# Kernel optimization log

Hardware: AMD Instinct MI355X
Metric: run time of the kernel (lower is better)

## Reference

```python
import jax, jax.numpy as jnp
import numpy as np

B, N, NFEAT = 64, 384, 16
E = 3
NHID, NOUT = 128, 128
ST_HID, ST_OUT = 64, 16


def _xavier(key, shape, fan_in, fan_out):
    a = jnp.sqrt(6.0 / (fan_in + fan_out))
    return jax.random.uniform(key, shape, jnp.float32, -a, a)


def setup_inputs() -> dict:
    key = jax.random.key(0)
    ks = jax.random.split(key, 10)
    x = jax.random.normal(ks[0], (B, N, NFEAT), jnp.float32)
    adj = jax.random.uniform(ks[1], (B, E, N, N), jnp.float32)
    emb_w = _xavier(ks[2], (NFEAT, NFEAT), NFEAT, NFEAT)            # Linear(nfeat,nfeat,bias=False)
    gc1_w = _xavier(ks[3], (E, NFEAT, NHID), NFEAT, NHID)           # (edge_dim,in,out)
    gc2_w = _xavier(ks[4], (E, NHID, NHID), NHID, NHID)             # single middle layer (num_layers-2=1)
    gc3_w = _xavier(ks[5], (E, NHID, NOUT), NHID, NOUT)
    st_w1 = _xavier(ks[6], (ST_HID, NOUT), NOUT, ST_HID)            # nn.Linear stores (out,in)
    st_b1 = jnp.zeros((ST_HID,), jnp.float32)
    st_w2 = jnp.full((2 * ST_OUT, ST_HID), 1e-10, jnp.float32)      # init.constant_(linear2.weight, 1e-10)
    st_b2 = jnp.zeros((2 * ST_OUT,), jnp.float32)
    rescale_w = jnp.zeros((1,), jnp.float32)                        # Rescale weight init zero
    return {"x": x, "adj": adj, "emb_w": emb_w, "gc1_w": gc1_w, "gc2_w": gc2_w,
            "gc3_w": gc3_w, "st_w1": st_w1, "st_b1": st_b1, "st_w2": st_w2,
            "st_b2": st_b2, "rescale_w": rescale_w}


def _rgcn_layer(h, adj, W, relu):
    # support: einsum('bid,edh->beih'), aggregate: einsum('beij,bejh->beih'), then sum over e
    support = jnp.einsum('bnd,edh->benh', h, W)
    out = jnp.einsum('bemn,benh->bemh', adj, support)
    if relu:
        out = jax.nn.relu(out)
    return out.sum(axis=1)  # aggregate='sum' over edge types


def reference(x, adj, emb_w, gc1_w, gc2_w, gc3_w, st_w1, st_b1, st_w2, st_b2, rescale_w):
    h = x @ emb_w.T                                   # emb Linear, no bias
    h = _rgcn_layer(h, adj, gc1_w, True)
    h = _rgcn_layer(h, adj, gc2_w, True)
    h = _rgcn_layer(h, adj, gc3_w, False)             # gc3: use_relu=False
    flat = h.reshape(-1, h.shape[-1])                 # (B*N, nout)
    z = jnp.tanh(flat @ st_w1.T + st_b1) @ st_w2.T + st_b2
    s, t = z[:, :ST_OUT], z[:, ST_OUT:]
    s = jnp.exp(rescale_w) * jnp.tanh(s)              # Rescale(tanh(s))
    return jnp.stack([s, t])                          # (2, B*N, ST_OUT)
```

## Files before the change

kernel.cpp:

```cpp
#include <hip/hip_runtime.h>
#include <math.h>

#define ROWS 24576
#define ADJ_BE (384*384)

typedef _Float16 h4v __attribute__((ext_vector_type(4)));
typedef _Float16 h8v __attribute__((ext_vector_type(8)));
typedef float f32x4 __attribute__((ext_vector_type(4)));

#define SPLIT_SCALE 2048.0f
#define INV_SPLIT_SCALE (1.0f / 2048.0f)

__global__ __launch_bounds__(256) void k_embed_adj(const float* __restrict__ x,
        const float* __restrict__ emb_w, const float* __restrict__ adj,
        float* __restrict__ T1) {
    __shared__ float h0L[384][16];
    __shared__ float aT[32][196];
    int t = threadIdx.x;
    int mt = blockIdx.x, e = blockIdx.y, b = blockIdx.z;
    float* embL = &aT[0][0];
    if (t < 64) *(float4*)&embL[4 * t] = *(const float4*)(emb_w + 4 * t);
    __syncthreads();
    const float* xb = x + (size_t)b * 384 * 16;
    for (int rr = t; rr < 384; rr += 256) {
        float xr[16];
        *(float4*)&xr[0]  = *(const float4*)(xb + rr * 16);
        *(float4*)&xr[4]  = *(const float4*)(xb + rr * 16 + 4);
        *(float4*)&xr[8]  = *(const float4*)(xb + rr * 16 + 8);
        *(float4*)&xr[12] = *(const float4*)(xb + rr * 16 + 12);
        float o[16];
#pragma unroll
        for (int d = 0; d < 16; ++d) {
            float acc = 0.f;
#pragma unroll
            for (int k = 0; k < 16; ++k) acc = fmaf(xr[k], embL[d * 16 + k], acc);
            o[d] = acc;
        }
        *(float4*)&h0L[rr][0]  = *(float4*)&o[0];
        *(float4*)&h0L[rr][4]  = *(float4*)&o[4];
        *(float4*)&h0L[rr][8]  = *(float4*)&o[8];
        *(float4*)&h0L[rr][12] = *(float4*)&o[12];
    }
    const float* A = adj + (size_t)(b * 3 + e) * ADJ_BE + (size_t)mt * 192 * 384;
    int tc = t & 3, ty = t >> 2;
    float acc[3][4] = {};
    for (int k0 = 0; k0 < 384; k0 += 32) {
        __syncthreads();
#pragma unroll
        for (int p = 0; p < 6; ++p) {
            int idx = t + p * 256;
            int r = idx >> 3, q = idx & 7;
            float4 v = *(const float4*)(A + (size_t)r * 384 + k0 + q * 4);
            aT[q*4+0][r] = v.x; aT[q*4+1][r] = v.y; aT[q*4+2][r] = v.z; aT[q*4+3][r] = v.w;
        }
        __syncthreads();
#pragma unroll
        for (int k = 0; k < 32; ++k) {
            float2 a01 = *(const float2*)&aT[k][2 * ty];
            float a2 = aT[k][128 + ty];
            float4 bv = *(const float4*)&h0L[k0 + k][4 * tc];
            float bb[4] = {bv.x, bv.y, bv.z, bv.w};
#pragma unroll
            for (int j = 0; j < 4; ++j) {
                acc[0][j] = fmaf(a01.x, bb[j], acc[0][j]);
                acc[1][j] = fmaf(a01.y, bb[j], acc[1][j]);
                acc[2][j] = fmaf(a2,    bb[j], acc[2][j]);
            }
        }
    }
    float* Tp = T1 + (size_t)(b * 3 + e) * (384 * 16) + (size_t)(mt * 192) * 16;
    *(float4*)&Tp[(2 * ty) * 16 + 4 * tc]     = make_float4(acc[0][0], acc[0][1], acc[0][2], acc[0][3]);
    *(float4*)&Tp[(2 * ty + 1) * 16 + 4 * tc] = make_float4(acc[1][0], acc[1][1], acc[1][2], acc[1][3]);
    *(float4*)&Tp[(128 + ty) * 16 + 4 * tc]   = make_float4(acc[2][0], acc[2][1], acc[2][2], acc[2][3]);
}

__global__ __launch_bounds__(256) void k_l1s2(const float* __restrict__ T1,
        const float* __restrict__ W1, float* __restrict__ h1) {
    __shared__ float wL[3][16][128];
    __shared__ float tL[3][64][17];
    int t = threadIdx.x;
    int rt = blockIdx.x;
    int b = rt / 6, m0 = (rt % 6) * 64;
#pragma unroll
    for (int p = 0; p < 6; ++p) {
        int idx = t + p * 256;
        float4 v = *(const float4*)(W1 + (size_t)idx * 4);
        int e = idx / 512, rem = idx % 512;
        int d = rem >> 5, q = rem & 31;
        *(float4*)&wL[e][d][q * 4] = v;
    }
#pragma unroll
    for (int p = 0; p < 3; ++p) {
        int idx = t + p * 256;
        int e = idx >> 8, rem = idx & 255;
        int r = rem >> 2, q = rem & 3;
        float4 v = *(const float4*)(T1 + ((size_t)(b * 3 + e) * 384 + m0 + r) * 16 + q * 4);
        tL[e][r][q*4+0] = v.x; tL[e][r][q*4+1] = v.y; tL[e][r][q*4+2] = v.z; tL[e][r][q*4+3] = v.w;
    }
    __syncthreads();
    int tx = t & 31;
    int ty = t >> 5;
    float tot[8][4] = {};
#pragma unroll
    for (int e = 0; e < 3; ++e) {
        float acc[8][4] = {};
#pragma unroll
        for (int d = 0; d < 16; ++d) {
            float a[8], w[4];
#pragma unroll
            for (int i = 0; i < 8; ++i) a[i] = tL[e][ty + 8 * i][d];
#pragma unroll
            for (int j = 0; j < 4; ++j) w[j] = wL[e][d][tx + 32 * j];
#pragma unroll
            for (int i = 0; i < 8; ++i)
#pragma unroll
                for (int j = 0; j < 4; ++j)
                    acc[i][j] = fmaf(a[i], w[j], acc[i][j]);
        }
#pragma unroll
        for (int i = 0; i < 8; ++i)
#pragma unroll
            for (int j = 0; j < 4; ++j)
                tot[i][j] += fmaxf(acc[i][j], 0.f);
    }
    float* out = h1 + (size_t)rt * 64 * 128;
#pragma unroll
    for (int i = 0; i < 8; ++i)
#pragma unroll
        for (int j = 0; j < 4; ++j)
            out[(ty + 8 * i) * 128 + tx + 32 * j] = tot[i][j];
}

__global__ __launch_bounds__(256) void k_support(const float* __restrict__ hin,
        const float* __restrict__ W, _Float16* __restrict__ Sh, _Float16* __restrict__ Sl) {
    int rt = blockIdx.x, e = blockIdx.y;
    int b = rt / 6, n0 = (rt % 6) * 64;
    const float* Hp = hin + (size_t)rt * 64 * 128;
    const float* Wp = W + (size_t)e * 128 * 128;
    __shared__ float aT[32][68];
    __shared__ float bT[32][132];
    int t = threadIdx.x;
    int tx = t & 15;
    int ty = t >> 4;
    float acc[4][8] = {};
    for (int k0 = 0; k0 < 128; k0 += 32) {
        __syncthreads();
#pragma unroll
        for (int p = 0; p < 2; ++p) {
            int idx = t + p * 256;
            int r = idx >> 3, q = idx & 7;
            float4 v = *(const float4*)(Hp + (size_t)r * 128 + k0 + q * 4);
            aT[q*4+0][r] = v.x; aT[q*4+1][r] = v.y; aT[q*4+2][r] = v.z; aT[q*4+3][r] = v.w;
        }
#pragma unroll
        for (int p = 0; p < 4; ++p) {
            int idx = t + p * 256;
            int r = idx >> 5, q = idx & 31;
            *(float4*)&bT[r][q * 4] = *(const float4*)(Wp + (size_t)(k0 + r) * 128 + q * 4);
        }
        __syncthreads();
#pragma unroll
        for (int k = 0; k < 32; ++k) {
            float4 av = *(const float4*)&aT[k][4 * ty];
            float4 b0 = *(const float4*)&bT[k][4 * tx];
            float4 b1 = *(const float4*)&bT[k][64 + 4 * tx];
            float a[4] = {av.x, av.y, av.z, av.w};
            float bb[8] = {b0.x, b0.y, b0.z, b0.w, b1.x, b1.y, b1.z, b1.w};
#pragma unroll
            for (int i = 0; i < 4; ++i)
#pragma unroll
                for (int j = 0; j < 8; ++j)
                    acc[i][j] = fmaf(a[i], bb[j], acc[i][j]);
        }
    }
    size_t base = (size_t)(b * 3 + e) * 128 * 384;
#pragma unroll
    for (int j = 0; j < 8; ++j) {
        int n = (j < 4) ? (4 * tx + j) : (64 + 4 * tx + j - 4);
        h4v hh, ll;
#pragma unroll
        for (int i = 0; i < 4; ++i) {
            float v = acc[i][j];
            _Float16 h = (_Float16)v;
            hh[i] = h;
            ll[i] = (_Float16)((v - (float)h) * SPLIT_SCALE);
        }
        size_t off = base + (size_t)n * 384 + n0 + 4 * ty;
        *(h4v*)(Sh + off) = hh;
        *(h4v*)(Sl + off) = ll;
    }
}

template <int RELU>
__global__ __launch_bounds__(256, 3) void k_adj_mfma(const float* __restrict__ adj,
        const _Float16* __restrict__ Sh, const _Float16* __restrict__ Sl,
        float* __restrict__ out) {
    int mt = blockIdx.x, e = blockIdx.y, b = blockIdx.z;
    const float* A = adj + (size_t)(b * 3 + e) * ADJ_BE + (size_t)mt * 96 * 384;
    const _Float16* Bh = Sh + (size_t)(b * 3 + e) * 128 * 384;
    const _Float16* Bl = Sl + (size_t)(b * 3 + e) * 128 * 384;
    float* O = out + ((size_t)b * 384 + mt * 96) * 128;

    __shared__ _Float16 Af[2][6][4][16][8];
    __shared__ _Float16 Bf[2][8][4][16][8];

    int t = threadIdx.x;
    int wave = t >> 6, lane = t & 63;
    int l16 = lane & 15, quad = lane >> 4;
    int wm = wave >> 1, wn = wave & 1;

    f32x4 acc0[3][4], acc1[3][4];
#pragma unroll
    for (int i = 0; i < 3; ++i)
#pragma unroll
        for (int j = 0; j < 4; ++j) {
            acc0[i][j] = f32x4{0.f, 0.f, 0.f, 0.f};
            acc1[i][j] = f32x4{0.f, 0.f, 0.f, 0.f};
        }

    for (int k0 = 0; k0 < 384; k0 += 32) {
        __syncthreads();
#pragma unroll
        for (int p = 0; p < 3; ++p) {
            int idx = t + p * 256;
            int r = idx >> 3, q4 = idx & 7;
            float4 v = *(const float4*)(A + (size_t)r * 384 + k0 + 4 * q4);
            h4v hh, ll;
            float vv[4] = {v.x, v.y, v.z, v.w};
#pragma unroll
            for (int c = 0; c < 4; ++c) {
                _Float16 h = (_Float16)vv[c];
                hh[c] = h;
                ll[c] = (_Float16)((vv[c] - (float)h) * SPLIT_SCALE);
            }
            *(h4v*)&Af[0][r >> 4][q4 >> 1][r & 15][(q4 & 1) * 4] = hh;
            *(h4v*)&Af[1][r >> 4][q4 >> 1][r & 15][(q4 & 1) * 4] = ll;
        }
#pragma unroll
        for (int p = 0; p < 2; ++p) {
            int idx = t + p * 256;
            int n = idx >> 2, q8 = idx & 3;
            size_t off = (size_t)n * 384 + k0 + 8 * q8;
            *(h8v*)&Bf[0][n >> 4][q8][n & 15][0] = *(const h8v*)(Bh + off);
            *(h8v*)&Bf[1][n >> 4][q8][n & 15][0] = *(const h8v*)(Bl + off);
        }
        __syncthreads();
        h8v a_h[3], a_l[3];
#pragma unroll
        for (int i = 0; i < 3; ++i) {
            a_h[i] = *(const h8v*)&Af[0][3 * wm + i][quad][l16][0];
            a_l[i] = *(const h8v*)&Af[1][3 * wm + i][quad][l16][0];
        }
#pragma unroll
        for (int j = 0; j < 4; ++j) {
            h8v b_h = *(const h8v*)&Bf[0][4 * wn + j][quad][l16][0];
            h8v b_l = *(const h8v*)&Bf[1][4 * wn + j][quad][l16][0];
#pragma unroll
            for (int i = 0; i < 3; ++i) {
                acc0[i][j] = __builtin_amdgcn_mfma_f32_16x16x32_f16(a_h[i], b_h, acc0[i][j], 0, 0, 0);
                acc1[i][j] = __builtin_amdgcn_mfma_f32_16x16x32_f16(a_h[i], b_l, acc1[i][j], 0, 0, 0);
                acc1[i][j] = __builtin_amdgcn_mfma_f32_16x16x32_f16(a_l[i], b_h, acc1[i][j], 0, 0, 0);
            }
        }
    }
#pragma unroll
    for (int i = 0; i < 3; ++i) {
        int r0 = 48 * wm + 16 * i + quad * 4;
#pragma unroll
        for (int j = 0; j < 4; ++j) {
            int gc = 64 * wn + 16 * j + l16;
#pragma unroll
            for (int reg = 0; reg < 4; ++reg) {
                float v = fmaf(acc1[i][j][reg], INV_SPLIT_SCALE, acc0[i][j][reg]);
                if (RELU) v = fmaxf(v, 0.f);
                atomicAdd(O + (size_t)(r0 + reg) * 128 + gc, v);
            }
        }
    }
}

__global__ void k_zero(float* __restrict__ p, int n4) {
    int i = blockIdx.x * blockDim.x + threadIdx.x;
    if (i < n4) ((float4*)p)[i] = float4{0.f, 0.f, 0.f, 0.f};
}

__global__ __launch_bounds__(256) void k_head(const float* __restrict__ h3,
        const float* __restrict__ st_w1, const float* __restrict__ st_b1,
        const float* __restrict__ st_w2, const float* __restrict__ st_b2,
        const float* __restrict__ rescale_w, float* __restrict__ out) {
    __shared__ float hL[64][132];
    __shared__ float w1L[64][132];
    __shared__ float ytL[64][68];
    __shared__ float w2L[32][68];
    __shared__ float b1L[64], b2L[32];
    int t = threadIdx.x;
    int r0 = blockIdx.x * 64;
#pragma unroll
    for (int p = 0; p < 8; ++p) {
        int idx = t + p * 256;
        int r = idx >> 5, q = idx & 31;
        *(float4*)&hL[r][q * 4] = *(const float4*)(h3 + (size_t)(r0 + r) * 128 + q * 4);
    }
#pragma unroll
    for (int p = 0; p < 8; ++p) {
        int idx = t + p * 256;
        int r = idx >> 5, q = idx & 31;
        *(float4*)&w1L[r][q * 4] = *(const float4*)(st_w1 + (size_t)r * 128 + q * 4);
    }
#pragma unroll
    for (int p = 0; p < 2; ++p) {
        int idx = t + p * 256;
        int r = idx >> 4, q = idx & 15;
        *(float4*)&w2L[r][q * 4] = *(const float4*)(st_w2 + (size_t)r * 64 + q * 4);
    }
    if (t < 64) b1L[t] = st_b1[t];
    else if (t < 96) b2L[t - 64] = st_b2[t - 64];
    __syncthreads();
    int tx = t & 15, ty = t >> 4;
    float acc[4][4] = {};
    for (int d = 0; d < 128; ++d) {
        float a[4], w[4];
#pragma unroll
        for (int i = 0; i < 4; ++i) a[i] = hL[ty + 16 * i][d];
#pragma unroll
        for (int j = 0; j < 4; ++j) w[j] = w1L[tx + 16 * j][d];
#pragma unroll
        for (int i = 0; i < 4; ++i)
#pragma unroll
            for (int j = 0; j < 4; ++j)
                acc[i][j] = fmaf(a[i], w[j], acc[i][j]);
    }
#pragma unroll
    for (int i = 0; i < 4; ++i)
#pragma unroll
        for (int j = 0; j < 4; ++j)
            ytL[ty + 16 * i][tx + 16 * j] = tanhf(acc[i][j] + b1L[tx + 16 * j]);
    __syncthreads();
    int tx8 = t & 7, ty32 = t >> 3;
    float acc2[2][4] = {};
    for (int d = 0; d < 64; ++d) {
        float a[2], w[4];
#pragma unroll
        for (int i = 0; i < 2; ++i) a[i] = ytL[ty32 + 32 * i][d];
#pragma unroll
        for (int j = 0; j < 4; ++j) w[j] = w2L[tx8 + 8 * j][d];
#pragma unroll
        for (int i = 0; i < 2; ++i)
#pragma unroll
            for (int j = 0; j < 4; ++j)
                acc2[i][j] = fmaf(a[i], w[j], acc2[i][j]);
    }
    float er = expf(rescale_w[0]);
#pragma unroll
    for (int i = 0; i < 2; ++i) {
        int r = r0 + ty32 + 32 * i;
#pragma unroll
        for (int j = 0; j < 4; ++j) {
            int c = tx8 + 8 * j;
            float z = acc2[i][j] + b2L[c];
            if (c < 16) out[(size_t)r * 16 + c] = er * tanhf(z);
            else        out[(size_t)(ROWS + r) * 16 + (c - 16)] = z;
        }
    }
}

extern "C" void kernel_launch(void* const* d_in, const int* in_sizes, int n_in,
                              void* d_out, int out_size, void* d_ws, size_t ws_size,
                              hipStream_t stream) {
    const float* x     = (const float*)d_in[0];
    const float* adj   = (const float*)d_in[1];
    const float* emb_w = (const float*)d_in[2];
    const float* gc1   = (const float*)d_in[3];
    const float* gc2   = (const float*)d_in[4];
    const float* gc3   = (const float*)d_in[5];
    const float* st_w1 = (const float*)d_in[6];
    const float* st_b1 = (const float*)d_in[7];
    const float* st_w2 = (const float*)d_in[8];
    const float* st_b2 = (const float*)d_in[9];
    const float* resc  = (const float*)d_in[10];
    float* out = (float*)d_out;
    float* ws  = (float*)d_ws;

    float* T1 = ws;
    float* hA = T1 + 1179648;
    float* hB = hA + 3145728;
    _Float16* Sh = (_Float16*)(hB + 3145728);
    _Float16* Sl = Sh + 9437184;

    k_embed_adj<<<dim3(2, 3, 64), 256, 0, stream>>>(x, emb_w, adj, T1);
    k_l1s2<<<384, 256, 0, stream>>>(T1, gc1, hA);
    k_support<<<dim3(384, 3), 256, 0, stream>>>(hA, gc2, Sh, Sl);
    k_zero<<<3072, 256, 0, stream>>>(hB, 786432);
    k_adj_mfma<1><<<dim3(4, 3, 64), 256, 0, stream>>>(adj, Sh, Sl, hB);
    k_support<<<dim3(384, 3), 256, 0, stream>>>(hB, gc3, Sh, Sl);
    k_zero<<<3072, 256, 0, stream>>>(hA, 786432);
    k_adj_mfma<0><<<dim3(4, 3, 64), 256, 0, stream>>>(adj, Sh, Sl, hA);
    k_head<<<384, 256, 0, stream>>>(hA, st_w1, st_b1, st_w2, st_b2, resc, out);
}
```

Before: 456.5 us.

## Fold embedding into layer-1 weights and run layer 1 through MFMA adjacency kernel

Precomputes emb_w^T·W1 per edge type so layer-1 support comes directly from x, then reuses the split-FP16 MFMA adjacency kernel for layer 1 instead of the FP32 adj·h0 kernel followed by a small GEMM. It also adds a fourth lo×lo MFMA term to the adjacency product for extra accuracy. This drops the separate FP32 adjacency pass and T1 buffer, but makes the layer-1 adjacency product 128 wide instead of 16 wide, and adds MFMA work to every adjacency pass.

```diff
diff --git a/kernel.cpp b/kernel.cpp
--- a/kernel.cpp
+++ b/kernel.cpp
@@ -11,124 +11,81 @@
 #define SPLIT_SCALE 2048.0f
 #define INV_SPLIT_SCALE (1.0f / 2048.0f)
 
-__global__ __launch_bounds__(256) void k_embed_adj(const float* __restrict__ x,
-        const float* __restrict__ emb_w, const float* __restrict__ adj,
-        float* __restrict__ T1) {
-    __shared__ float h0L[384][16];
-    __shared__ float aT[32][196];
-    int t = threadIdx.x;
-    int mt = blockIdx.x, e = blockIdx.y, b = blockIdx.z;
-    float* embL = &aT[0][0];
-    if (t < 64) *(float4*)&embL[4 * t] = *(const float4*)(emb_w + 4 * t);
+__global__ __launch_bounds__(256) void k_prep(const float* __restrict__ emb_w,
+        const float* __restrict__ W1, float* __restrict__ M1) {
+    __shared__ float embL[16][16];
+    int t = threadIdx.x;
+    embL[t >> 4][t & 15] = emb_w[t];
     __syncthreads();
-    const float* xb = x + (size_t)b * 384 * 16;
-    for (int rr = t; rr < 384; rr += 256) {
-        float xr[16];
-        *(float4*)&xr[0]  = *(const float4*)(xb + rr * 16);
-        *(float4*)&xr[4]  = *(const float4*)(xb + rr * 16 + 4);
-        *(float4*)&xr[8]  = *(const float4*)(xb + rr * 16 + 8);
-        *(float4*)&xr[12] = *(const float4*)(xb + rr * 16 + 12);
-        float o[16];
-#pragma unroll
-        for (int d = 0; d < 16; ++d) {
+    int c = t & 127, half = t >> 7;
+#pragma unroll
+    for (int e = 0; e < 3; ++e) {
+        float w[16];
+#pragma unroll
+        for (int f = 0; f < 16; ++f) w[f] = W1[(size_t)(e * 16 + f) * 128 + c];
+#pragma unroll
+        for (int dd = 0; dd < 8; ++dd) {
+            int d = half * 8 + dd;
             float acc = 0.f;
 #pragma unroll
-            for (int k = 0; k < 16; ++k) acc = fmaf(xr[k], embL[d * 16 + k], acc);
-            o[d] = acc;
-        }
-        *(float4*)&h0L[rr][0]  = *(float4*)&o[0];
-        *(float4*)&h0L[rr][4]  = *(float4*)&o[4];
-        *(float4*)&h0L[rr][8]  = *(float4*)&o[8];
-        *(float4*)&h0L[rr][12] = *(float4*)&o[12];
-    }
-    const float* A = adj + (size_t)(b * 3 + e) * ADJ_BE + (size_t)mt * 192 * 384;
-    int tc = t & 3, ty = t >> 2;
-    float acc[3][4] = {};
-    for (int k0 = 0; k0 < 384; k0 += 32) {
-        __syncthreads();
-#pragma unroll
-        for (int p = 0; p < 6; ++p) {
-            int idx = t + p * 256;
-            int r = idx >> 3, q = idx & 7;
-            float4 v = *(const float4*)(A + (size_t)r * 384 + k0 + q * 4);
-            aT[q*4+0][r] = v.x; aT[q*4+1][r] = v.y; aT[q*4+2][r] = v.z; aT[q*4+3][r] = v.w;
-        }
-        __syncthreads();
-#pragma unroll
-        for (int k = 0; k < 32; ++k) {
-            float2 a01 = *(const float2*)&aT[k][2 * ty];
-            float a2 = aT[k][128 + ty];
-            float4 bv = *(const float4*)&h0L[k0 + k][4 * tc];
-            float bb[4] = {bv.x, bv.y, bv.z, bv.w};
-#pragma unroll
-            for (int j = 0; j < 4; ++j) {
-                acc[0][j] = fmaf(a01.x, bb[j], acc[0][j]);
-                acc[1][j] = fmaf(a01.y, bb[j], acc[1][j]);
-                acc[2][j] = fmaf(a2,    bb[j], acc[2][j]);
-            }
-        }
-    }
-    float* Tp = T1 + (size_t)(b * 3 + e) * (384 * 16) + (size_t)(mt * 192) * 16;
-    *(float4*)&Tp[(2 * ty) * 16 + 4 * tc]     = make_float4(acc[0][0], acc[0][1], acc[0][2], acc[0][3]);
-    *(float4*)&Tp[(2 * ty + 1) * 16 + 4 * tc] = make_float4(acc[1][0], acc[1][1], acc[1][2], acc[1][3]);
-    *(float4*)&Tp[(128 + ty) * 16 + 4 * tc]   = make_float4(acc[2][0], acc[2][1], acc[2][2], acc[2][3]);
-}
-
-__global__ __launch_bounds__(256) void k_l1s2(const float* __restrict__ T1,
-        const float* __restrict__ W1, float* __restrict__ h1) {
-    __shared__ float wL[3][16][128];
-    __shared__ float tL[3][64][17];
-    int t = threadIdx.x;
-    int rt = blockIdx.x;
-    int b = rt / 6, m0 = (rt % 6) * 64;
-#pragma unroll
-    for (int p = 0; p < 6; ++p) {
+            for (int f = 0; f < 16; ++f) acc = fmaf(embL[f][d], w[f], acc);
+            M1[(size_t)(e * 16 + d) * 128 + c] = acc;
+        }
+    }
+}
+
+__global__ __launch_bounds__(256) void k_support16(const float* __restrict__ x,
+        const float* __restrict__ M1, _Float16* __restrict__ Sh, _Float16* __restrict__ Sl) {
+    int rt = blockIdx.x, e = blockIdx.y;
+    int b = rt / 6, n0 = (rt % 6) * 64;
+    const float* Xp = x + (size_t)rt * 64 * 16;
+    const float* Mp = M1 + (size_t)e * 16 * 128;
+    __shared__ float xT[16][68];
+    __shared__ float mB[16][132];
+    int t = threadIdx.x;
+    {
+        int r = t >> 2, q = t & 3;
+        float4 v = *(const float4*)(Xp + (size_t)r * 16 + q * 4);
+        xT[q*4+0][r] = v.x; xT[q*4+1][r] = v.y; xT[q*4+2][r] = v.z; xT[q*4+3][r] = v.w;
+    }
+#pragma unroll
+    for (int p = 0; p < 2; ++p) {
         int idx = t + p * 256;
-        float4 v = *(const float4*)(W1 + (size_t)idx * 4);
-        int e = idx / 512, rem = idx % 512;
-        int d = rem >> 5, q = rem & 31;
-        *(float4*)&wL[e][d][q * 4] = v;
-    }
-#pragma unroll
-    for (int p = 0; p < 3; ++p) {
-        int idx = t + p * 256;
-        int e = idx >> 8, rem = idx & 255;
-        int r = rem >> 2, q = rem & 3;
-        float4 v = *(const float4*)(T1 + ((size_t)(b * 3 + e) * 384 + m0 + r) * 16 + q * 4);
-        tL[e][r][q*4+0] = v.x; tL[e][r][q*4+1] = v.y; tL[e][r][q*4+2] = v.z; tL[e][r][q*4+3] = v.w;
+        int r = idx >> 5, q = idx & 31;
+        *(float4*)&mB[r][q * 4] = *(const float4*)(Mp + (size_t)r * 128 + q * 4);
     }
     __syncthreads();
-    int tx = t & 31;
-    int ty = t >> 5;
-    float tot[8][4] = {};
-#pragma unroll
-    for (int e = 0; e < 3; ++e) {
-        float acc[8][4] = {};
-#pragma unroll
-        for (int d = 0; d < 16; ++d) {
-            float a[8], w[4];
-#pragma unroll
-            for (int i = 0; i < 8; ++i) a[i] = tL[e][ty + 8 * i][d];
-#pragma unroll
-            for (int j = 0; j < 4; ++j) w[j] = wL[e][d][tx + 32 * j];
-#pragma unroll
-            for (int i = 0; i < 8; ++i)
-#pragma unroll
-                for (int j = 0; j < 4; ++j)
-                    acc[i][j] = fmaf(a[i], w[j], acc[i][j]);
-        }
-#pragma unroll
-        for (int i = 0; i < 8; ++i)
-#pragma unroll
-            for (int j = 0; j < 4; ++j)
-                tot[i][j] += fmaxf(acc[i][j], 0.f);
-    }
-    float* out = h1 + (size_t)rt * 64 * 128;
-#pragma unroll
-    for (int i = 0; i < 8; ++i)
-#pragma unroll
-        for (int j = 0; j < 4; ++j)
-            out[(ty + 8 * i) * 128 + tx + 32 * j] = tot[i][j];
+    int tx = t & 15, ty = t >> 4;
+    float acc[4][8] = {};
+#pragma unroll
+    for (int k = 0; k < 16; ++k) {
+        float4 av = *(const float4*)&xT[k][4 * ty];
+        float4 b0 = *(const float4*)&mB[k][4 * tx];
+        float4 b1 = *(const float4*)&mB[k][64 + 4 * tx];
+        float a[4] = {av.x, av.y, av.z, av.w};
+        float bb[8] = {b0.x, b0.y, b0.z, b0.w, b1.x, b1.y, b1.z, b1.w};
+#pragma unroll
+        for (int i = 0; i < 4; ++i)
+#pragma unroll
+            for (int j = 0; j < 8; ++j)
+                acc[i][j] = fmaf(a[i], bb[j], acc[i][j]);
+    }
+    size_t base = (size_t)(b * 3 + e) * 128 * 384;
+#pragma unroll
+    for (int j = 0; j < 8; ++j) {
+        int n = (j < 4) ? (4 * tx + j) : (64 + 4 * tx + j - 4);
+        h4v hh, ll;
+#pragma unroll
+        for (int i = 0; i < 4; ++i) {
+            float v = acc[i][j];
+            _Float16 h = (_Float16)v;
+            hh[i] = h;
+            ll[i] = (_Float16)((v - (float)h) * SPLIT_SCALE);
+        }
+        size_t off = base + (size_t)n * 384 + n0 + 4 * ty;
+        *(h4v*)(Sh + off) = hh;
+        *(h4v*)(Sl + off) = ll;
+    }
 }
 
 __global__ __launch_bounds__(256) void k_support(const float* __restrict__ hin,
@@ -245,11 +202,12 @@
             *(h8v*)&Bf[1][n >> 4][q8][n & 15][0] = *(const h8v*)(Bl + off);
         }
         __syncthreads();
-        h8v a_h[3], a_l[3];
+        h8v a_h[3], a_l[3], a_d[3];
 #pragma unroll
         for (int i = 0; i < 3; ++i) {
             a_h[i] = *(const h8v*)&Af[0][3 * wm + i][quad][l16][0];
             a_l[i] = *(const h8v*)&Af[1][3 * wm + i][quad][l16][0];
+            a_d[i] = a_l[i] * (_Float16)INV_SPLIT_SCALE;
         }
 #pragma unroll
         for (int j = 0; j < 4; ++j) {
@@ -260,6 +218,7 @@
                 acc0[i][j] = __builtin_amdgcn_mfma_f32_16x16x32_f16(a_h[i], b_h, acc0[i][j], 0, 0, 0);
                 acc1[i][j] = __builtin_amdgcn_mfma_f32_16x16x32_f16(a_h[i], b_l, acc1[i][j], 0, 0, 0);
                 acc1[i][j] = __builtin_amdgcn_mfma_f32_16x16x32_f16(a_l[i], b_h, acc1[i][j], 0, 0, 0);
+                acc1[i][j] = __builtin_amdgcn_mfma_f32_16x16x32_f16(a_d[i], b_l, acc1[i][j], 0, 0, 0);
             }
         }
     }
@@ -381,14 +340,16 @@
     float* out = (float*)d_out;
     float* ws  = (float*)d_ws;
 
-    float* T1 = ws;
-    float* hA = T1 + 1179648;
+    float* M1 = ws;
+    float* hA = M1 + 6144;
     float* hB = hA + 3145728;
     _Float16* Sh = (_Float16*)(hB + 3145728);
     _Float16* Sl = Sh + 9437184;
 
-    k_embed_adj<<<dim3(2, 3, 64), 256, 0, stream>>>(x, emb_w, adj, T1);
-    k_l1s2<<<384, 256, 0, stream>>>(T1, gc1, hA);
+    k_prep<<<1, 256, 0, stream>>>(emb_w, gc1, M1);
+    k_support16<<<dim3(384, 3), 256, 0, stream>>>(x, M1, Sh, Sl);
+    k_zero<<<3072, 256, 0, stream>>>(hA, 786432);
+    k_adj_mfma<1><<<dim3(4, 3, 64), 256, 0, stream>>>(adj, Sh, Sl, hA);
     k_support<<<dim3(384, 3), 256, 0, stream>>>(hA, gc2, Sh, Sl);
     k_zero<<<3072, 256, 0, stream>>>(hB, 786432);
     k_adj_mfma<1><<<dim3(4, 3, 64), 256, 0, stream>>>(adj, Sh, Sl, hB);
```

After: 475.2 us. +4.1%, slower.
